# Optimization experiments

Measured on AMD Instinct MI355X. Metric: run time of the kernel, lower is better.

## Reference

```python
import jax, jax.numpy as jnp
import numpy as np
from jax import lax

B, T, C = 64, 1024, 256


def setup_inputs() -> dict:
    key = jax.random.key(0)
    k1, k2 = jax.random.split(key)
    sequences = jax.random.normal(k1, (B, T, C), dtype=jnp.float32)
    transitions = jax.random.normal(k2, (C, C), dtype=jnp.float32)
    return {"sequences": sequences, "transitions": transitions}


def _viterbi_decode(sequences, transitions):
    # sequences: [B, T, C] unary scores; transitions: [C_prev, C_cur]
    num_classes = sequences.shape[-1]
    emissions = jnp.swapaxes(sequences, 0, 1)  # [T, B, C]

    def fwd_step(alpha, emit):
        # alpha: [B, C_prev]; emit: [B, C_cur]
        m = alpha[:, :, None] + transitions[None, :, :]  # [B, C_prev, C_cur]
        bp = jnp.argmax(m, axis=1).astype(jnp.int32)     # [B, C_cur] backpointers
        new_alpha = jnp.max(m, axis=1) + emit            # [B, C_cur]
        return new_alpha, bp

    alpha, bps = lax.scan(fwd_step, emissions[0], emissions[1:])  # bps: [T-1, B, C]
    last_tag = jnp.argmax(alpha, axis=-1).astype(jnp.int32)       # [B]

    def back_step(tag, bp):
        # tag: [B] tag at t+1; bp: [B, C] backpointers computed at step t+1
        prev = jnp.take_along_axis(bp, tag[:, None], axis=1)[:, 0]
        return prev, prev

    _, tags = lax.scan(back_step, last_tag, bps, reverse=True)  # [T-1, B]
    full = jnp.concatenate([tags, last_tag[None, :]], axis=0)   # [T, B]
    return jnp.swapaxes(full, 0, 1)  # [B, T]


def reference(sequences, transitions):
    # Inference path of CRF.call: viterbi decode + one-hot over num_classes.
    tags = _viterbi_decode(sequences, transitions)
    return jax.nn.one_hot(tags, sequences.shape[-1], dtype=sequences.dtype)
```

## Files before the change

kernel.cpp:

```cpp
#include <hip/hip_runtime.h>

#define Bn 64
#define Tn 1024
#define Cn 256

template<int CTRL>
__device__ __forceinline__ float dpp_mov_f(float x) {
  return __int_as_float(__builtin_amdgcn_update_dpp(0, __float_as_int(x), CTRL, 0xF, 0xF, true));
}
template<int CTRL>
__device__ __forceinline__ void max_stage(float& v) {
  const float pv = __int_as_float(__builtin_amdgcn_update_dpp(
      (int)0xFF800000, __float_as_int(v), CTRL, 0xF, 0xF, false));
  v = fmaxf(v, pv);
}

__device__ __forceinline__ int argmax64_fast(float v, int i) {
  float mv = v;
  max_stage<0x111>(mv);
  max_stage<0x112>(mv);
  max_stage<0x114>(mv);
  max_stage<0x118>(mv);
  max_stage<0x142>(mv);
  max_stage<0x143>(mv);
  const float smax = __int_as_float(__builtin_amdgcn_readlane(__float_as_int(mv), 63));
  const unsigned long long m = __ballot(v == smax);
  const int ln = __ffsll((unsigned long long)m) - 1;
  return __builtin_amdgcn_readlane(i, ln);
}

__device__ __forceinline__ int apad(int m) { return (m >> 2) * 20 + (m & 3) * 4; }

template<int K, int PK>
__device__ __forceinline__ void fwd_chunk(
    int tb, float* __restrict__ sb, int ccb, bool leader, int c,
    float* ab0, float* ab1, int woff0, int woff1, const float4* tr4,
    float4 (&e)[4][2], float4 (&na)[4][2]) {
  if (leader) {
#pragma unroll
    for (int k = 0; k < PK; ++k) {
      *(float4*)(sb + (size_t)(tb - PK + k) * Cn + ccb) = na[k][0];
      *(float4*)(sb + (size_t)(tb - PK + k) * Cn + ccb + 4) = na[k][1];
    }
#pragma unroll
    for (int k = 0; k < K; ++k) {
      e[k][0] = *(const float4*)(sb + (size_t)(tb + k) * Cn + ccb);
      e[k][1] = *(const float4*)(sb + (size_t)(tb + k) * Cn + ccb + 4);
    }
  }
#pragma unroll
  for (int k = 0; k < K; ++k) {
    const int t = tb + k;
    const float* av = (t & 1) ? ab0 : ab1;
    float* aw = (t & 1) ? ab1 : ab0;
    const float* avc = av + c * 20;
    float m0 = -__builtin_inff(), m1 = m0, m2 = m0, m3 = m0,
          m4 = m0, m5 = m0, m6 = m0, m7 = m0;
#pragma unroll
    for (int j = 0; j < 4; ++j) {
      const float4 a = *(const float4*)(avc + 4 * j);
#define STEP8(av_, kk)                                                            \
      {                                                                           \
        const float4 tA = tr4[(kk) * 2 + 0];                                      \
        const float4 tB = tr4[(kk) * 2 + 1];                                      \
        m0 = fmaxf(m0, (av_) + tA.x); m1 = fmaxf(m1, (av_) + tA.y);               \
        m2 = fmaxf(m2, (av_) + tA.z); m3 = fmaxf(m3, (av_) + tA.w);               \
        m4 = fmaxf(m4, (av_) + tB.x); m5 = fmaxf(m5, (av_) + tB.y);               \
        m6 = fmaxf(m6, (av_) + tB.z); m7 = fmaxf(m7, (av_) + tB.w);               \
      }
      STEP8(a.x, 4 * j + 0)
      STEP8(a.y, 4 * j + 1)
      STEP8(a.z, 4 * j + 2)
      STEP8(a.w, 4 * j + 3)
#undef STEP8
    }
#define ROR8(CTRL)                                                                \
    m0 = fmaxf(m0, dpp_mov_f<CTRL>(m0)); m1 = fmaxf(m1, dpp_mov_f<CTRL>(m1));     \
    m2 = fmaxf(m2, dpp_mov_f<CTRL>(m2)); m3 = fmaxf(m3, dpp_mov_f<CTRL>(m3));     \
    m4 = fmaxf(m4, dpp_mov_f<CTRL>(m4)); m5 = fmaxf(m5, dpp_mov_f<CTRL>(m5));     \
    m6 = fmaxf(m6, dpp_mov_f<CTRL>(m6)); m7 = fmaxf(m7, dpp_mov_f<CTRL>(m7));
    ROR8(0x128) ROR8(0x124) ROR8(0x122) ROR8(0x121)
#undef ROR8
    if (leader) {
      float4 n0, n1;
      n0.x = m0 + e[k][0].x; n0.y = m1 + e[k][0].y;
      n0.z = m2 + e[k][0].z; n0.w = m3 + e[k][0].w;
      n1.x = m4 + e[k][1].x; n1.y = m5 + e[k][1].y;
      n1.z = m6 + e[k][1].z; n1.w = m7 + e[k][1].w;
      *(float4*)(aw + woff0) = n0;
      *(float4*)(aw + woff1) = n1;
      na[k][0] = n0; na[k][1] = n1;
    }
    __syncthreads();
  }
}

__global__ __launch_bounds__(512, 2) void crf_fwd_kernel(
    float* __restrict__ seq, const float* __restrict__ trans,
    float* __restrict__ transT, int useT) {
  __shared__ float lds[64 * 65];
  const int bi = blockIdx.x;
  const int tid = threadIdx.x;

  if (bi < Bn) {
    float* sb = seq + (size_t)bi * (Tn * Cn);
    const int l = tid & 63;
    const int w = tid >> 6;
    const int c = l & 15;
    const int g = l >> 4;
    const int ccb = w * 32 + g * 8;
    const int cpb = c * 16;
    float4 tr4[32];
#pragma unroll
    for (int k = 0; k < 16; ++k) {
      tr4[2 * k + 0] = *(const float4*)(trans + (size_t)(cpb + k) * Cn + ccb);
      tr4[2 * k + 1] = *(const float4*)(trans + (size_t)(cpb + k) * Cn + ccb + 4);
    }
    float* ab0 = lds;
    float* ab1 = lds + 320;
    if (tid < 64) *(float4*)(ab0 + apad(tid)) = ((const float4*)sb)[tid];
    const bool leader = (c == 0);
    const int m0c = w * 8 + g * 2;
    const int woff0 = apad(m0c), woff1 = apad(m0c + 1);
    float4 e[4][2], na[4][2];
    __syncthreads();

    fwd_chunk<3, 0>(1, sb, ccb, leader, c, ab0, ab1, woff0, woff1, tr4, e, na);
    fwd_chunk<4, 3>(4, sb, ccb, leader, c, ab0, ab1, woff0, woff1, tr4, e, na);
    for (int tb = 8; tb < Tn; tb += 4)
      fwd_chunk<4, 4>(tb, sb, ccb, leader, c, ab0, ab1, woff0, woff1, tr4, e, na);
    if (leader) {
#pragma unroll
      for (int k = 0; k < 4; ++k) {
        *(float4*)(sb + (size_t)(1020 + k) * Cn + ccb) = na[k][0];
        *(float4*)(sb + (size_t)(1020 + k) * Cn + ccb + 4) = na[k][1];
      }
    }
  } else if (useT) {
    const int idx = bi - Bn;
    const int ti = idx >> 2, tj = idx & 3;
    const int tx = tid & 63, ty = tid >> 6;
#pragma unroll
    for (int q = 0; q < 8; ++q) {
      const int row = q * 8 + ty;
      lds[tx * 65 + row] = trans[(size_t)(ti * 64 + row) * Cn + tj * 64 + tx];
    }
    __syncthreads();
#pragma unroll
    for (int q = 0; q < 8; ++q) {
      const int row = q * 8 + ty;
      transT[(size_t)(tj * 64 + row) * Cn + ti * 64 + tx] = lds[row * 65 + tx];
    }
  }
}

__device__ __forceinline__ float4 onehot4(int tg, int cp0) {
  float4 z;
  z.x = (tg == cp0 + 0) ? 1.0f : 0.0f; z.y = (tg == cp0 + 1) ? 1.0f : 0.0f;
  z.z = (tg == cp0 + 2) ? 1.0f : 0.0f; z.w = (tg == cp0 + 3) ? 1.0f : 0.0f;
  return z;
}

template<int K>
__device__ __forceinline__ int chain_chunk(
    const float* __restrict__ A, int* __restrict__ tags,
    const float* __restrict__ transT, int tag, int l) {
  const int cp0 = l * 4;
#pragma unroll
  for (int k = 0; k < K; ++k) {
    const float4 tv = *(const float4*)(transT + (size_t)tag * Cn + cp0);
    const float4 ac = *(const float4*)(A + k * Cn + cp0);
    float v = ac.x + tv.x; int i = cp0;
    float vv; bool cnd;
    vv = ac.y + tv.y; cnd = vv > v; v = cnd ? vv : v; i = cnd ? cp0 + 1 : i;
    vv = ac.z + tv.z; cnd = vv > v; v = cnd ? vv : v; i = cnd ? cp0 + 2 : i;
    vv = ac.w + tv.w; cnd = vv > v; v = cnd ? vv : v; i = cnd ? cp0 + 3 : i;
    tag = argmax64_fast(v, i);
    if (l == 0) tags[k] = tag;
  }
  return tag;
}

__global__ __launch_bounds__(256) void crf_bwd_kernel(
    const float* __restrict__ seq, const float* __restrict__ trans,
    const float* __restrict__ transT, float* __restrict__ out, int useT) {
  __shared__ float aL[2][16][Cn];
  __shared__ int tagL[2][16];
  const int b = blockIdx.x;
  const int tid = threadIdx.x;
  const int wv = tid >> 6;
  const int l = tid & 63;
  const int cp0 = l * 4;
  const float* sb = seq + (size_t)b * (Tn * Cn);
  float* ob = out + (size_t)b * (Tn * Cn);

  if (!useT) {
    if (wv == 0) {
      float4 a = *(const float4*)(sb + (size_t)(Tn - 1) * Cn + cp0);
      float v = a.x; int i = cp0; bool cnd;
      cnd = a.y > v; v = cnd ? a.y : v; i = cnd ? cp0 + 1 : i;
      cnd = a.z > v; v = cnd ? a.z : v; i = cnd ? cp0 + 2 : i;
      cnd = a.w > v; v = cnd ? a.w : v; i = cnd ? cp0 + 3 : i;
      int tag = argmax64_fast(v, i);
      *(float4*)(ob + (size_t)(Tn - 1) * Cn + cp0) = onehot4(tag, cp0);
      for (int t = Tn - 2; t >= 0; --t) {
        const float4 ac = *(const float4*)(sb + (size_t)t * Cn + cp0);
        float4 tv;
        tv.x = trans[(size_t)(cp0 + 0) * Cn + tag];
        tv.y = trans[(size_t)(cp0 + 1) * Cn + tag];
        tv.z = trans[(size_t)(cp0 + 2) * Cn + tag];
        tv.w = trans[(size_t)(cp0 + 3) * Cn + tag];
        float v2 = ac.x + tv.x; int i2 = cp0; float vv; bool c2;
        vv = ac.y + tv.y; c2 = vv > v2; v2 = c2 ? vv : v2; i2 = c2 ? cp0 + 1 : i2;
        vv = ac.z + tv.z; c2 = vv > v2; v2 = c2 ? vv : v2; i2 = c2 ? cp0 + 2 : i2;
        vv = ac.w + tv.w; c2 = vv > v2; v2 = c2 ? vv : v2; i2 = c2 ? cp0 + 3 : i2;
        tag = argmax64_fast(v2, i2);
        *(float4*)(ob + (size_t)t * Cn + cp0) = onehot4(tag, cp0);
      }
    }
    return;
  }

  int tag = 0;
  if (wv == 0) {
    float4 a = *(const float4*)(sb + (size_t)(Tn - 1) * Cn + cp0);
    float v = a.x; int i = cp0; bool cnd;
    cnd = a.y > v; v = cnd ? a.y : v; i = cnd ? cp0 + 1 : i;
    cnd = a.z > v; v = cnd ? a.z : v; i = cnd ? cp0 + 2 : i;
    cnd = a.w > v; v = cnd ? a.w : v; i = cnd ? cp0 + 3 : i;
    tag = argmax64_fast(v, i);
    *(float4*)(ob + (size_t)(Tn - 1) * Cn + cp0) = onehot4(tag, cp0);
  } else if (wv <= 2) {
    const int s0 = (wv == 1) ? 0 : 8, s1 = (wv == 1) ? 8 : 15;
    for (int s = s0; s < s1; ++s)
      *(float4*)(&aL[0][s][cp0]) = *(const float4*)(sb + (size_t)(1022 - s) * Cn + cp0);
  }
  __syncthreads();

  int p = 0, t0 = 1022, K = 15, pt0 = 0, pK = 0;
  for (int ch = 0; ch < 64; ++ch) {
    const int nt0 = t0 - K;
    if (wv == 0) {
      if (ch == 0) tag = chain_chunk<15>(&aL[p][0][0], tagL[p], transT, tag, l);
      else        tag = chain_chunk<16>(&aL[p][0][0], tagL[p], transT, tag, l);
    } else if (wv <= 2) {
      if (ch < 63) {
        const int s0 = (wv == 1) ? 0 : 8, s1 = (wv == 1) ? 8 : 16;
        for (int s = s0; s < s1; ++s)
          *(float4*)(&aL[1 - p][s][cp0]) =
              *(const float4*)(sb + (size_t)(nt0 - s) * Cn + cp0);
      }
    } else {
      if (ch > 0) {
        for (int k = 0; k < pK; ++k)
          *(float4*)(ob + (size_t)(pt0 - k) * Cn + cp0) =
              onehot4(tagL[1 - p][k], cp0);
      }
    }
    __syncthreads();
    pt0 = t0; pK = K; t0 = nt0; K = 16; p ^= 1;
  }
  if (wv == 3) {
    for (int k = 0; k < 16; ++k)
      *(float4*)(ob + (size_t)(15 - k) * Cn + cp0) = onehot4(tagL[1][k], cp0);
  }
}

extern "C" void kernel_launch(void* const* d_in, const int* in_sizes, int n_in,
                              void* d_out, int out_size, void* d_ws, size_t ws_size,
                              hipStream_t stream) {
  float* seq = (float*)d_in[0];
  const float* trans = (const float*)d_in[1];
  float* out = (float*)d_out;
  float* transT = (float*)d_ws;
  const int useT = (ws_size >= (size_t)Cn * Cn * sizeof(float)) ? 1 : 0;

  crf_fwd_kernel<<<dim3(Bn + 16), dim3(512), 0, stream>>>(seq, trans, transT, useT);
  crf_bwd_kernel<<<dim3(Bn), dim3(256), 0, stream>>>(seq, trans, transT, out, useT);
}
```

Baseline: 1.449 ms.

## Double forward block to 1024 threads with 4 columns per thread, per-step prefetch

```diff
diff --git a/kernel.cpp b/kernel.cpp
--- a/kernel.cpp
+++ b/kernel.cpp
@@ -3,6 +3,14 @@
 #define Bn 64
 #define Tn 1024
 #define Cn 256
+
+#define FWD_SYNC()                                  \
+  do {                                              \
+    __builtin_amdgcn_sched_barrier(0);              \
+    __builtin_amdgcn_s_waitcnt(0xC07F);             \
+    __builtin_amdgcn_s_barrier();                   \
+    __builtin_amdgcn_sched_barrier(0);              \
+  } while (0)
 
 template<int CTRL>
 __device__ __forceinline__ float dpp_mov_f(float x) {
@@ -31,71 +39,7 @@
 
 __device__ __forceinline__ int apad(int m) { return (m >> 2) * 20 + (m & 3) * 4; }
 
-template<int K, int PK>
-__device__ __forceinline__ void fwd_chunk(
-    int tb, float* __restrict__ sb, int ccb, bool leader, int c,
-    float* ab0, float* ab1, int woff0, int woff1, const float4* tr4,
-    float4 (&e)[4][2], float4 (&na)[4][2]) {
-  if (leader) {
-#pragma unroll
-    for (int k = 0; k < PK; ++k) {
-      *(float4*)(sb + (size_t)(tb - PK + k) * Cn + ccb) = na[k][0];
-      *(float4*)(sb + (size_t)(tb - PK + k) * Cn + ccb + 4) = na[k][1];
-    }
-#pragma unroll
-    for (int k = 0; k < K; ++k) {
-      e[k][0] = *(const float4*)(sb + (size_t)(tb + k) * Cn + ccb);
-      e[k][1] = *(const float4*)(sb + (size_t)(tb + k) * Cn + ccb + 4);
-    }
-  }
-#pragma unroll
-  for (int k = 0; k < K; ++k) {
-    const int t = tb + k;
-    const float* av = (t & 1) ? ab0 : ab1;
-    float* aw = (t & 1) ? ab1 : ab0;
-    const float* avc = av + c * 20;
-    float m0 = -__builtin_inff(), m1 = m0, m2 = m0, m3 = m0,
-          m4 = m0, m5 = m0, m6 = m0, m7 = m0;
-#pragma unroll
-    for (int j = 0; j < 4; ++j) {
-      const float4 a = *(const float4*)(avc + 4 * j);
-#define STEP8(av_, kk)                                                            \
-      {                                                                           \
-        const float4 tA = tr4[(kk) * 2 + 0];                                      \
-        const float4 tB = tr4[(kk) * 2 + 1];                                      \
-        m0 = fmaxf(m0, (av_) + tA.x); m1 = fmaxf(m1, (av_) + tA.y);               \
-        m2 = fmaxf(m2, (av_) + tA.z); m3 = fmaxf(m3, (av_) + tA.w);               \
-        m4 = fmaxf(m4, (av_) + tB.x); m5 = fmaxf(m5, (av_) + tB.y);               \
-        m6 = fmaxf(m6, (av_) + tB.z); m7 = fmaxf(m7, (av_) + tB.w);               \
-      }
-      STEP8(a.x, 4 * j + 0)
-      STEP8(a.y, 4 * j + 1)
-      STEP8(a.z, 4 * j + 2)
-      STEP8(a.w, 4 * j + 3)
-#undef STEP8
-    }
-#define ROR8(CTRL)                                                                \
-    m0 = fmaxf(m0, dpp_mov_f<CTRL>(m0)); m1 = fmaxf(m1, dpp_mov_f<CTRL>(m1));     \
-    m2 = fmaxf(m2, dpp_mov_f<CTRL>(m2)); m3 = fmaxf(m3, dpp_mov_f<CTRL>(m3));     \
-    m4 = fmaxf(m4, dpp_mov_f<CTRL>(m4)); m5 = fmaxf(m5, dpp_mov_f<CTRL>(m5));     \
-    m6 = fmaxf(m6, dpp_mov_f<CTRL>(m6)); m7 = fmaxf(m7, dpp_mov_f<CTRL>(m7));
-    ROR8(0x128) ROR8(0x124) ROR8(0x122) ROR8(0x121)
-#undef ROR8
-    if (leader) {
-      float4 n0, n1;
-      n0.x = m0 + e[k][0].x; n0.y = m1 + e[k][0].y;
-      n0.z = m2 + e[k][0].z; n0.w = m3 + e[k][0].w;
-      n1.x = m4 + e[k][1].x; n1.y = m5 + e[k][1].y;
-      n1.z = m6 + e[k][1].z; n1.w = m7 + e[k][1].w;
-      *(float4*)(aw + woff0) = n0;
-      *(float4*)(aw + woff1) = n1;
-      na[k][0] = n0; na[k][1] = n1;
-    }
-    __syncthreads();
-  }
-}
-
-__global__ __launch_bounds__(512, 2) void crf_fwd_kernel(
+__global__ __launch_bounds__(1024) void crf_fwd_kernel(
     float* __restrict__ seq, const float* __restrict__ trans,
     float* __restrict__ transT, int useT) {
   __shared__ float lds[64 * 65];
@@ -108,47 +52,80 @@
     const int w = tid >> 6;
     const int c = l & 15;
     const int g = l >> 4;
-    const int ccb = w * 32 + g * 8;
+    const int ccb = w * 16 + g * 4;
     const int cpb = c * 16;
-    float4 tr4[32];
-#pragma unroll
-    for (int k = 0; k < 16; ++k) {
-      tr4[2 * k + 0] = *(const float4*)(trans + (size_t)(cpb + k) * Cn + ccb);
-      tr4[2 * k + 1] = *(const float4*)(trans + (size_t)(cpb + k) * Cn + ccb + 4);
-    }
+    float4 tr4[16];
+#pragma unroll
+    for (int k = 0; k < 16; ++k)
+      tr4[k] = *(const float4*)(trans + (size_t)(cpb + k) * Cn + ccb);
+
     float* ab0 = lds;
     float* ab1 = lds + 320;
     if (tid < 64) *(float4*)(ab0 + apad(tid)) = ((const float4*)sb)[tid];
     const bool leader = (c == 0);
-    const int m0c = w * 8 + g * 2;
-    const int woff0 = apad(m0c), woff1 = apad(m0c + 1);
-    float4 e[4][2], na[4][2];
-    __syncthreads();
-
-    fwd_chunk<3, 0>(1, sb, ccb, leader, c, ab0, ab1, woff0, woff1, tr4, e, na);
-    fwd_chunk<4, 3>(4, sb, ccb, leader, c, ab0, ab1, woff0, woff1, tr4, e, na);
-    for (int tb = 8; tb < Tn; tb += 4)
-      fwd_chunk<4, 4>(tb, sb, ccb, leader, c, ab0, ab1, woff0, woff1, tr4, e, na);
-    if (leader) {
-#pragma unroll
-      for (int k = 0; k < 4; ++k) {
-        *(float4*)(sb + (size_t)(1020 + k) * Cn + ccb) = na[k][0];
-        *(float4*)(sb + (size_t)(1020 + k) * Cn + ccb + 4) = na[k][1];
-      }
-    }
+    const int woff = apad(w * 4 + g);
+    float4 e4, pna;
+    if (leader) e4 = *(const float4*)(sb + Cn + ccb);
+    FWD_SYNC();
+
+    for (int t = 1; t < Tn; ++t) {
+      float4 pf;
+      if (leader) {
+        if (t > 1) *(float4*)(sb + (size_t)(t - 1) * Cn + ccb) = pna;
+        const int tn = (t + 1 < Tn) ? (t + 1) : (Tn - 1);
+        pf = *(const float4*)(sb + (size_t)tn * Cn + ccb);
+      }
+      const float* av = (t & 1) ? ab0 : ab1;
+      float* aw = (t & 1) ? ab1 : ab0;
+      const float* avc = av + c * 20;
+      float m0 = -__builtin_inff(), m1 = m0, m2 = m0, m3 = m0;
+#pragma unroll
+      for (int j = 0; j < 4; ++j) {
+        const float4 a = *(const float4*)(avc + j * 4);
+        float4 t0 = tr4[4 * j + 0];
+        m0 = fmaxf(m0, a.x + t0.x); m1 = fmaxf(m1, a.x + t0.y);
+        m2 = fmaxf(m2, a.x + t0.z); m3 = fmaxf(m3, a.x + t0.w);
+        float4 t1 = tr4[4 * j + 1];
+        m0 = fmaxf(m0, a.y + t1.x); m1 = fmaxf(m1, a.y + t1.y);
+        m2 = fmaxf(m2, a.y + t1.z); m3 = fmaxf(m3, a.y + t1.w);
+        float4 t2 = tr4[4 * j + 2];
+        m0 = fmaxf(m0, a.z + t2.x); m1 = fmaxf(m1, a.z + t2.y);
+        m2 = fmaxf(m2, a.z + t2.z); m3 = fmaxf(m3, a.z + t2.w);
+        float4 t3 = tr4[4 * j + 3];
+        m0 = fmaxf(m0, a.w + t3.x); m1 = fmaxf(m1, a.w + t3.y);
+        m2 = fmaxf(m2, a.w + t3.z); m3 = fmaxf(m3, a.w + t3.w);
+      }
+      m0 = fmaxf(m0, dpp_mov_f<0x128>(m0)); m1 = fmaxf(m1, dpp_mov_f<0x128>(m1));
+      m2 = fmaxf(m2, dpp_mov_f<0x128>(m2)); m3 = fmaxf(m3, dpp_mov_f<0x128>(m3));
+      m0 = fmaxf(m0, dpp_mov_f<0x124>(m0)); m1 = fmaxf(m1, dpp_mov_f<0x124>(m1));
+      m2 = fmaxf(m2, dpp_mov_f<0x124>(m2)); m3 = fmaxf(m3, dpp_mov_f<0x124>(m3));
+      m0 = fmaxf(m0, dpp_mov_f<0x122>(m0)); m1 = fmaxf(m1, dpp_mov_f<0x122>(m1));
+      m2 = fmaxf(m2, dpp_mov_f<0x122>(m2)); m3 = fmaxf(m3, dpp_mov_f<0x122>(m3));
+      m0 = fmaxf(m0, dpp_mov_f<0x121>(m0)); m1 = fmaxf(m1, dpp_mov_f<0x121>(m1));
+      m2 = fmaxf(m2, dpp_mov_f<0x121>(m2)); m3 = fmaxf(m3, dpp_mov_f<0x121>(m3));
+      if (leader) {
+        float4 na;
+        na.x = m0 + e4.x; na.y = m1 + e4.y; na.z = m2 + e4.z; na.w = m3 + e4.w;
+        *(float4*)(aw + woff) = na;
+        pna = na;
+        e4 = pf;
+      }
+      FWD_SYNC();
+    }
+    if (leader) *(float4*)(sb + (size_t)(Tn - 1) * Cn + ccb) = pna;
   } else if (useT) {
     const int idx = bi - Bn;
     const int ti = idx >> 2, tj = idx & 3;
     const int tx = tid & 63, ty = tid >> 6;
 #pragma unroll
-    for (int q = 0; q < 8; ++q) {
-      const int row = q * 8 + ty;
+    for (int q = 0; q < 4; ++q) {
+      const int row = q * 16 + ty;
       lds[tx * 65 + row] = trans[(size_t)(ti * 64 + row) * Cn + tj * 64 + tx];
     }
     __syncthreads();
 #pragma unroll
-    for (int q = 0; q < 8; ++q) {
-      const int row = q * 8 + ty;
+    for (int q = 0; q < 4; ++q) {
+      const int row = q * 16 + ty;
       transT[(size_t)(tj * 64 + row) * Cn + ti * 64 + tx] = lds[row * 65 + tx];
     }
   }
@@ -275,6 +252,6 @@
   float* transT = (float*)d_ws;
   const int useT = (ws_size >= (size_t)Cn * Cn * sizeof(float)) ? 1 : 0;
 
-  crf_fwd_kernel<<<dim3(Bn + 16), dim3(512), 0, stream>>>(seq, trans, transT, useT);
+  crf_fwd_kernel<<<dim3(Bn + 16), dim3(1024), 0, stream>>>(seq, trans, transT, useT);
   crf_bwd_kernel<<<dim3(Bn), dim3(256), 0, stream>>>(seq, trans, transT, out, useT);
 }
```

New measurement: 1.309 ms. 9.6% less time.
